# Kernel tuning notes

Measured on AMD Instinct MI355X. Metric: run time of the kernel, lower is better.

## Reference

```python
import jax, jax.numpy as jnp
import numpy as np

B, S, DM = 2, 2048, 2048
H, KV, HD = 16, 4, 128
THETA = 10000.0
EPS = 1e-6


def _rmsnorm(x, scale):
    # flax nnx.RMSNorm with dtype=float32: x / sqrt(mean(x^2)+eps) * scale
    var = jnp.mean(jnp.square(x.astype(jnp.float32)), axis=-1, keepdims=True)
    return (x.astype(jnp.float32) * jax.lax.rsqrt(var + EPS)) * scale


def _apply_rope(x, positions, base):
    # x: [B, S, heads, HD]; positions: [1, S]
    half = HD // 2
    fraction = 2.0 * jnp.arange(half, dtype=jnp.float32) / HD
    timescale = base ** fraction                              # [HD/2]
    sinusoid = positions[..., None].astype(jnp.float32) / timescale  # [1, S, HD/2]
    sinusoid = sinusoid[..., None, :]                         # [1, S, 1, HD/2]
    sin, cos = jnp.sin(sinusoid), jnp.cos(sinusoid)
    x1, x2 = x[..., :half], x[..., half:]
    return jnp.concatenate([x1 * cos - x2 * sin, x2 * cos + x1 * sin], axis=-1).astype(x.dtype)


def setup_inputs() -> dict:
    key = jax.random.key(0)
    ks = jax.random.split(key, 7)
    w = lambda k, shape: jax.random.normal(k, shape, jnp.float32) * 0.02
    return {
        "x": jax.random.normal(ks[0], (B, S, DM), jnp.float32),
        "wq": w(ks[1], (DM, H, HD)),
        "wk": w(ks[2], (DM, KV, HD)),
        "wv": w(ks[3], (DM, KV, HD)),
        "wo": w(ks[4], (H, HD, DM)),
        "q_scale": jnp.ones((HD,), jnp.float32),
        "k_scale": jnp.ones((HD,), jnp.float32),
    }


def reference(x, wq, wk, wv, wo, q_scale, k_scale):
    # QKV projections (LinearGeneral hidden -> (heads, head_dim))
    q = jnp.einsum("bsd,dhk->bshk", x, wq)   # [B,S,H,HD]
    k = jnp.einsum("bsd,dhk->bshk", x, wk)   # [B,S,KV,HD]
    v = jnp.einsum("bsd,dhk->bshk", x, wv)   # [B,S,KV,HD]
    # qk RMSNorm + cast back to compute dtype
    q = _rmsnorm(q, q_scale).astype(x.dtype)
    k = _rmsnorm(k, k_scale).astype(x.dtype)
    # RoPE
    positions = jnp.arange(S)[None, :]
    q = _apply_rope(q, positions, THETA)
    k = _apply_rope(k, positions, THETA)
    # GQA attention: group query heads per kv head instead of materializing repeat_kv
    G = H // KV
    qg = q.reshape(B, S, KV, G, HD) * (HD ** -0.5)
    scores = jnp.einsum("bqkgd,bskd->bkgqs", qg, k)           # [B,KV,G,S,S]
    causal = jnp.tril(jnp.ones((S, S), jnp.bool_))
    scores = jnp.where(causal, scores, jnp.finfo(scores.dtype).min)
    probs = jax.nn.softmax(scores, axis=-1)
    att = jnp.einsum("bkgqs,bskd->bqkgd", probs, v).reshape(B, S, H, HD)
    # output projection contracting (heads, head_dim)
    return jnp.einsum("bshd,hdo->bso", att, wo)
```

## Files before the change

### kernel.cpp

```cpp
#include <hip/hip_runtime.h>
#include <hip/hip_bf16.h>
#include <math.h>

typedef unsigned short u16;
typedef short short8 __attribute__((ext_vector_type(8)));
typedef float floatx4 __attribute__((ext_vector_type(4)));

#define B_   2
#define S_   2048
#define DM_  2048
#define H_   16
#define KVH_ 4
#define HD_  128

__device__ __forceinline__ float bf2f(u16 v) {
  union { unsigned int u; float f; } x; x.u = ((unsigned int)v) << 16; return x.f;
}
__device__ __forceinline__ u16 f2bf(float f) {
  union { float f; unsigned int u; } x; x.f = f;
  unsigned int u = x.u;
  u += 0x7FFFu + ((u >> 16) & 1u);
  return (u16)(u >> 16);
}

#define GLDS16(gp, lp) __builtin_amdgcn_global_load_lds( \
    (const __attribute__((address_space(1))) unsigned int*)(const void*)(gp), \
    (__attribute__((address_space(3))) unsigned int*)(void*)(lp), 16, 0, 0)

__global__ __launch_bounds__(256) void k_prep(
    const float* __restrict__ x, const float* __restrict__ wq,
    const float* __restrict__ wk, const float* __restrict__ wv,
    const float* __restrict__ wo,
    u16* __restrict__ x_bf, u16* __restrict__ wqkv_t, u16* __restrict__ wo_t)
{
  int bx = blockIdx.x;
  if (bx < 8192) {
    int i = bx * 256 + threadIdx.x;
    const float4 v = ((const float4*)x)[i];
    u16 o[4] = { f2bf(v.x), f2bf(v.y), f2bf(v.z), f2bf(v.w) };
    *(unsigned long long*)(x_bf + (size_t)i * 4) = *(unsigned long long*)o;
    return;
  }
  bx -= 8192;
  const float* src; u16* dst; int C, cb;
  if (bx < 4096)      { src = wq; dst = wqkv_t; C = 2048; cb = 64; }
  else if (bx < 5120) { bx -= 4096; src = wk; dst = wqkv_t + (size_t)2048 * 2048; C = 512; cb = 16; }
  else if (bx < 6144) { bx -= 5120; src = wv; dst = wqkv_t + (size_t)2560 * 2048; C = 512; cb = 16; }
  else                { bx -= 6144; src = wo; dst = wo_t; C = 2048; cb = 64; }
  const int R = 2048;
  int c0 = (bx % cb) * 32, r0 = (bx / cb) * 32;
  __shared__ float tile[32][33];
  int tx = threadIdx.x & 31, ty = threadIdx.x >> 5;
#pragma unroll
  for (int j = 0; j < 4; j++)
    tile[ty * 4 + j][tx] = src[(size_t)(r0 + ty * 4 + j) * C + c0 + tx];
  __syncthreads();
#pragma unroll
  for (int j = 0; j < 4; j++)
    dst[(size_t)(c0 + ty * 4 + j) * R + r0 + tx] = f2bf(tile[tx][ty * 4 + j]);
}

__global__ __launch_bounds__(256, 3) void k_gemm_bt(
    const u16* __restrict__ A, const u16* __restrict__ Bt,
    void* __restrict__ Cout, int M, int N, int K, int c_bf16)
{
  __shared__ u16 As[128 * 64];
  __shared__ u16 Bs[128 * 64];
  int tid = threadIdx.x;
  int lane = tid & 63;
  int quad = lane >> 4, l16 = lane & 15;
  int wid = tid >> 6;
  int m0 = blockIdx.y * 128, n0 = blockIdx.x * 128;
  int wm = (wid >> 1) * 64, wn = (wid & 1) * 64;

  floatx4 acc[4][4] = {};

  int srow = tid >> 3;
  int gjc0 = (tid & 7) ^ (srow & 7);
  const u16* Ap = A + (size_t)(m0 + srow) * K + gjc0 * 8;
  const u16* Bp = Bt + (size_t)(n0 + srow) * K + gjc0 * 8;
  u16* AsW = As + tid * 8;
  u16* BsW = Bs + tid * 8;

  for (int kt = 0; kt < K; kt += 64) {
    __syncthreads();
#pragma unroll
    for (int j = 0; j < 4; j++) {
      GLDS16(Ap + (size_t)(j * 32) * K, AsW + j * 2048);
      GLDS16(Bp + (size_t)(j * 32) * K, BsW + j * 2048);
    }
    Ap += 64; Bp += 64;
    __syncthreads();

#pragma unroll
    for (int ks = 0; ks < 2; ks++) {
      short8 af[4], bfv[4];
#pragma unroll
      for (int mi = 0; mi < 4; mi++) {
        int row = wm + mi * 16 + l16;
        af[mi] = *(const short8*)&As[row * 64 + (((ks * 4 + quad) ^ (row & 7)) * 8)];
      }
#pragma unroll
      for (int ni = 0; ni < 4; ni++) {
        int row = wn + ni * 16 + l16;
        bfv[ni] = *(const short8*)&Bs[row * 64 + (((ks * 4 + quad) ^ (row & 7)) * 8)];
      }
#pragma unroll
      for (int mi = 0; mi < 4; mi++)
#pragma unroll
        for (int ni = 0; ni < 4; ni++)
          acc[mi][ni] = __builtin_amdgcn_mfma_f32_16x16x32_bf16(
              af[mi], bfv[ni], acc[mi][ni], 0, 0, 0);
    }
  }

#pragma unroll
  for (int mi = 0; mi < 4; mi++)
#pragma unroll
    for (int ni = 0; ni < 4; ni++)
#pragma unroll
      for (int r = 0; r < 4; r++) {
        int row = m0 + wm + mi * 16 + quad * 4 + r;
        int col = n0 + wn + ni * 16 + l16;
        float v = acc[mi][ni][r];
        if (c_bf16) ((u16*)Cout)[(size_t)row * N + col] = f2bf(v);
        else        ((float*)Cout)[(size_t)row * N + col] = v;
      }
}

__global__ __launch_bounds__(256) void k_post(
    const u16* __restrict__ C1, const float* __restrict__ qs,
    const float* __restrict__ ks, u16* __restrict__ qr, u16* __restrict__ kr,
    u16* __restrict__ vt)
{
  int bx = blockIdx.x;
  if (bx < 4096) {
    int m = bx;
    int lane = threadIdx.x & 63, wid = threadIdx.x >> 6;
    int pos = m & (S_ - 1);
    float ts = powf(10000.0f, (float)lane * (1.0f / 64.0f));
    float ang = (float)pos / ts;
    float sn = sinf(ang), cs = cosf(ang);
    for (int r = wid; r < H_ + KVH_; r += 4) {
      bool isq = r < H_;
      const u16* src = C1 + (size_t)m * 3072 + (isq ? r * HD_ : DM_ + (r - H_) * HD_);
      float x1 = bf2f(src[lane]), x2 = bf2f(src[lane + 64]);
      float ss = x1 * x1 + x2 * x2;
#pragma unroll
      for (int d = 1; d < 64; d <<= 1) ss += __shfl_xor(ss, d);
      float rs = rsqrtf(ss * (1.0f / 128.0f) + 1e-6f);
      const float* sc = isq ? qs : ks;
      float y1 = x1 * rs * sc[lane];
      float y2 = x2 * rs * sc[lane + 64];
      float o1 = y1 * cs - y2 * sn;
      float o2 = y2 * cs + y1 * sn;
      if (isq) { o1 *= 0.088388347648318447f; o2 *= 0.088388347648318447f; }
      u16* dst = isq ? (qr + ((size_t)m * H_ + r) * HD_)
                     : (kr + ((size_t)m * KVH_ + (r - H_)) * HD_);
      dst[lane]      = f2bf(o1);
      dst[lane + 64] = f2bf(o2);
    }
    return;
  }
  bx -= 4096;
  int sx = bx & 63, rest = bx >> 6;
  int hy = rest & 3, bk = rest >> 2;
  int s0 = sx * 32, h0 = hy * 32;
  int b = bk >> 2, kv = bk & 3;
  __shared__ u16 tile[32][33];
  int tx = threadIdx.x & 31, ty = threadIdx.x >> 5;
#pragma unroll
  for (int j = 0; j < 4; j++)
    tile[ty * 4 + j][tx] =
        C1[(size_t)(b * S_ + s0 + ty * 4 + j) * 3072 + 2560 + kv * HD_ + h0 + tx];
  __syncthreads();
#pragma unroll
  for (int j = 0; j < 4; j++)
    vt[((size_t)bk * HD_ + h0 + ty * 4 + j) * S_ + s0 + tx] = tile[tx][ty * 4 + j];
}

__global__ __launch_bounds__(256, 2) void k_flash(
    const u16* __restrict__ qr, const u16* __restrict__ kr,
    const u16* __restrict__ vt, u16* __restrict__ att)
{
  __shared__ u16 Ks[64 * 128];
  __shared__ u16 Vt[128 * 64];
  __shared__ u16 Ps[4][32 * 64];
  int tid = threadIdx.x, lane = tid & 63, wid = tid >> 6;
  int quad = lane >> 4, l16 = lane & 15;
  int bx = blockIdx.x;
  int qi = 15 - (bx >> 5);
  int hb = bx & 31;
  int h = hb & 15, b = hb >> 4;
  int kvh = h >> 2;
  int q0 = qi * 128;
  int NT = 2 * qi + 2;
  int ktd = 2 * qi + (wid >> 1);

  short8 qf[2][4];
#pragma unroll
  for (int m = 0; m < 2; m++) {
    const u16* qb = qr + ((size_t)(b * S_ + q0 + wid * 32 + m * 16 + l16) * H_ + h) * HD_;
#pragma unroll
    for (int kk = 0; kk < 4; kk++)
      qf[m][kk] = *(const short8*)(qb + kk * 32 + quad * 8);
  }

  int gjk = (tid & 15) ^ ((tid >> 4) & 15);
  int gjv = (tid & 7) ^ ((tid >> 3) & 7);
  const u16* kp = kr + ((size_t)(b * S_ + (tid >> 4)) * KVH_ + kvh) * HD_ + gjk * 8;
  const u16* vp = vt + ((size_t)(b * KVH_ + kvh) * HD_ + (tid >> 3)) * S_ + gjv * 8;

  short8 pk[4], pv[4];
#pragma unroll
  for (int j = 0; j < 4; j++) {
    pk[j] = *(const short8*)(kp + (size_t)(j * 16) * KVH_ * HD_);
    pv[j] = *(const short8*)(vp + (size_t)(j * 32) * S_);
  }

  floatx4 accO[2][8] = {};
  float lp[2][4] = {};
  u16* PsW = &Ps[wid][0];

  const float LOG2E = 1.4426950408889634f;
  const float MBIAS = -12.5f * 1.4426950408889634f;

  for (int kt = 0; kt < NT; kt++) {
    int k0 = kt * 64;
#pragma unroll
    for (int j = 0; j < 4; j++) {
      *(short8*)&Ks[(j * 256 + tid) * 8] = pk[j];
      *(short8*)&Vt[(j * 256 + tid) * 8] = pv[j];
    }
    __syncthreads();

    if (kt + 1 < NT) {
      kp += (size_t)64 * KVH_ * HD_;
      vp += 64;
#pragma unroll
      for (int j = 0; j < 4; j++) {
        pk[j] = *(const short8*)(kp + (size_t)(j * 16) * KVH_ * HD_);
        pv[j] = *(const short8*)(vp + (size_t)(j * 32) * S_);
      }
    }

    if (kt <= ktd) {
      floatx4 sacc[2][4] = {};
      __builtin_amdgcn_s_setprio(1);
#pragma unroll
      for (int kk = 0; kk < 4; kk++) {
        short8 kf[4];
#pragma unroll
        for (int nt = 0; nt < 4; nt++) {
          int row = nt * 16 + l16;
          kf[nt] = *(const short8*)&Ks[row * 128 + (((kk * 4 + quad) ^ (row & 15)) * 8)];
        }
#pragma unroll
        for (int nt = 0; nt < 4; nt++) {
          sacc[0][nt] = __builtin_amdgcn_mfma_f32_16x16x32_bf16(qf[0][kk], kf[nt], sacc[0][nt], 0, 0, 0);
          sacc[1][nt] = __builtin_amdgcn_mfma_f32_16x16x32_bf16(qf[1][kk], kf[nt], sacc[1][nt], 0, 0, 0);
        }
      }
      __builtin_amdgcn_s_setprio(0);

      bool diag = (kt == ktd);
#pragma unroll
      for (int m = 0; m < 2; m++)
#pragma unroll
        for (int r = 0; r < 4; r++) {
          int prow = m * 16 + quad * 4 + r;
          int qrow = q0 + wid * 32 + prow;
          float rsum = 0.f;
#pragma unroll
          for (int nt = 0; nt < 4; nt++) {
            float p = __builtin_amdgcn_exp2f(fmaf(sacc[m][nt][r], LOG2E, MBIAS));
            if (diag && (k0 + nt * 16 + l16) > qrow) p = 0.f;
            rsum += p;
            PsW[prow * 64 + (((nt * 2 + (l16 >> 3)) ^ (prow & 7)) * 8) + (l16 & 7)] = f2bf(p);
          }
          lp[m][r] += rsum;
        }

      __builtin_amdgcn_s_setprio(1);
#pragma unroll
      for (int kk = 0; kk < 2; kk++) {
        short8 pf[2];
#pragma unroll
        for (int m = 0; m < 2; m++) {
          int prow = m * 16 + l16;
          pf[m] = *(const short8*)&PsW[prow * 64 + (((kk * 4 + quad) ^ (prow & 7)) * 8)];
        }
#pragma unroll
        for (int ht = 0; ht < 8; ht++) {
          int row = ht * 16 + l16;
          short8 vf = *(const short8*)&Vt[row * 64 + (((kk * 4 + quad) ^ (row & 7)) * 8)];
          accO[0][ht] = __builtin_amdgcn_mfma_f32_16x16x32_bf16(pf[0], vf, accO[0][ht], 0, 0, 0);
          accO[1][ht] = __builtin_amdgcn_mfma_f32_16x16x32_bf16(pf[1], vf, accO[1][ht], 0, 0, 0);
        }
      }
      __builtin_amdgcn_s_setprio(0);
    }
    __syncthreads();
  }

#pragma unroll
  for (int m = 0; m < 2; m++)
#pragma unroll
    for (int r = 0; r < 4; r++) {
#pragma unroll
      for (int d = 1; d < 16; d <<= 1) lp[m][r] += __shfl_xor(lp[m][r], d);
      lp[m][r] = 1.0f / lp[m][r];
    }

#pragma unroll
  for (int m = 0; m < 2; m++)
#pragma unroll
    for (int ht = 0; ht < 8; ht++)
#pragma unroll
      for (int r = 0; r < 4; r++) {
        int row = q0 + wid * 32 + m * 16 + quad * 4 + r;
        att[((size_t)(b * S_ + row) * H_ + h) * HD_ + ht * 16 + l16] =
            f2bf(accO[m][ht][r] * lp[m][r]);
      }
}

extern "C" void kernel_launch(void* const* d_in, const int* in_sizes, int n_in,
                              void* d_out, int out_size, void* d_ws, size_t ws_size,
                              hipStream_t stream)
{
  const float* x  = (const float*)d_in[0];
  const float* wq = (const float*)d_in[1];
  const float* wk = (const float*)d_in[2];
  const float* wv = (const float*)d_in[3];
  const float* wo = (const float*)d_in[4];
  const float* qs = (const float*)d_in[5];
  const float* ks = (const float*)d_in[6];

  char* ws = (char*)d_ws;
  size_t off = 0;
  u16* x_bf   = (u16*)(ws + off); off += (size_t)4096 * 2048 * 2;
  u16* wqkv_t = (u16*)(ws + off); off += (size_t)3072 * 2048 * 2;
  u16* wo_t   = (u16*)(ws + off); off += (size_t)2048 * 2048 * 2;
  u16* C1     = (u16*)(ws + off); off += (size_t)4096 * 3072 * 2;
  u16* q_rope = (u16*)(ws + off); off += (size_t)4096 * 16 * 128 * 2;
  u16* k_rope = (u16*)(ws + off); off += (size_t)4096 * 4 * 128 * 2;
  u16* vt     = (u16*)(ws + off); off += (size_t)8 * 128 * 2048 * 2;
  u16* att    = (u16*)(ws + off); off += (size_t)4096 * 2048 * 2;

  k_prep<<<dim3(18432), 256, 0, stream>>>(x, wq, wk, wv, wo, x_bf, wqkv_t, wo_t);

  k_gemm_bt<<<dim3(24, 32), 256, 0, stream>>>(x_bf, wqkv_t, C1, 4096, 3072, 2048, 1);

  k_post<<<dim3(6144), 256, 0, stream>>>(C1, qs, ks, q_rope, k_rope, vt);

  k_flash<<<dim3(512), 256, 0, stream>>>(q_rope, k_rope, vt, att);

  k_gemm_bt<<<dim3(16, 32), 256, 0, stream>>>(att, wo_t, d_out, 4096, 2048, 2048, 0);

  (void)in_sizes; (void)n_in; (void)out_size; (void)ws_size;
}
```

Before: 302.9 us.

## Split flash key tiles across wave pairs with double-buffered direct-to-LDS loads

The attention kernel now processes 64-row query tiles, giving twice as many blocks. The four waves split into two row halves by two key halves, and the split-K partial outputs and row sums are combined through shared memory at the end. K/V tiles are loaded with GLDS16 (global-to-LDS) into double buffers instead of through register staging, which removes one barrier per iteration. This aims at better load balance and occupancy across CUs and at hiding load latency, at the cost of more LDS and a final cross-wave reduction.

```diff
diff --git a/kernel.cpp b/kernel.cpp
--- a/kernel.cpp
+++ b/kernel.cpp
@@ -183,24 +183,26 @@
     const u16* __restrict__ qr, const u16* __restrict__ kr,
     const u16* __restrict__ vt, u16* __restrict__ att)
 {
-  __shared__ u16 Ks[64 * 128];
-  __shared__ u16 Vt[128 * 64];
-  __shared__ u16 Ps[4][32 * 64];
+  __shared__ u16 smem[39168] __attribute__((aligned(16)));
+  u16* Ps = smem + 32768;
+  float* lpbuf = (float*)(smem + 38912);
+
   int tid = threadIdx.x, lane = tid & 63, wid = tid >> 6;
   int quad = lane >> 4, l16 = lane & 15;
+  int rhalf = wid & 1;
+  int shalf = wid >> 1;
   int bx = blockIdx.x;
-  int qi = 15 - (bx >> 5);
+  int it = 31 - (bx >> 5);
   int hb = bx & 31;
   int h = hb & 15, b = hb >> 4;
   int kvh = h >> 2;
-  int q0 = qi * 128;
-  int NT = 2 * qi + 2;
-  int ktd = 2 * qi + (wid >> 1);
+  int q0 = it * 64;
+  int NT = it + 1;
 
   short8 qf[2][4];
 #pragma unroll
   for (int m = 0; m < 2; m++) {
-    const u16* qb = qr + ((size_t)(b * S_ + q0 + wid * 32 + m * 16 + l16) * H_ + h) * HD_;
+    const u16* qb = qr + ((size_t)(b * S_ + q0 + rhalf * 32 + m * 16 + l16) * H_ + h) * HD_;
 #pragma unroll
     for (int kk = 0; kk < 4; kk++)
       qf[m][kk] = *(const short8*)(qb + kk * 32 + quad * 8);
@@ -211,117 +213,145 @@
   const u16* kp = kr + ((size_t)(b * S_ + (tid >> 4)) * KVH_ + kvh) * HD_ + gjk * 8;
   const u16* vp = vt + ((size_t)(b * KVH_ + kvh) * HD_ + (tid >> 3)) * S_ + gjv * 8;
 
-  short8 pk[4], pv[4];
 #pragma unroll
   for (int j = 0; j < 4; j++) {
-    pk[j] = *(const short8*)(kp + (size_t)(j * 16) * KVH_ * HD_);
-    pv[j] = *(const short8*)(vp + (size_t)(j * 32) * S_);
-  }
+    GLDS16(kp + (size_t)(j * 16) * KVH_ * HD_, smem + (size_t)(j * 256 + tid) * 8);
+    GLDS16(vp + (size_t)(j * 32) * S_,         smem + 16384 + (size_t)(j * 256 + tid) * 8);
+  }
+  kp += (size_t)64 * KVH_ * HD_;
+  vp += 64;
+  __syncthreads();
 
   floatx4 accO[2][8] = {};
   float lp[2][4] = {};
-  u16* PsW = &Ps[wid][0];
+  u16* PsW = Ps + wid * 1536;
 
   const float LOG2E = 1.4426950408889634f;
   const float MBIAS = -12.5f * 1.4426950408889634f;
+  int qmax = q0 + rhalf * 32 + 31;
 
   for (int kt = 0; kt < NT; kt++) {
-    int k0 = kt * 64;
-#pragma unroll
-    for (int j = 0; j < 4; j++) {
-      *(short8*)&Ks[(j * 256 + tid) * 8] = pk[j];
-      *(short8*)&Vt[(j * 256 + tid) * 8] = pv[j];
-    }
-    __syncthreads();
-
     if (kt + 1 < NT) {
+      u16* KD = smem + (size_t)((kt + 1) & 1) * 8192;
+      u16* VD = smem + 16384 + (size_t)((kt + 1) & 1) * 8192;
+#pragma unroll
+      for (int j = 0; j < 4; j++) {
+        GLDS16(kp + (size_t)(j * 16) * KVH_ * HD_, KD + (size_t)(j * 256 + tid) * 8);
+        GLDS16(vp + (size_t)(j * 32) * S_,         VD + (size_t)(j * 256 + tid) * 8);
+      }
       kp += (size_t)64 * KVH_ * HD_;
       vp += 64;
-#pragma unroll
-      for (int j = 0; j < 4; j++) {
-        pk[j] = *(const short8*)(kp + (size_t)(j * 16) * KVH_ * HD_);
-        pv[j] = *(const short8*)(vp + (size_t)(j * 32) * S_);
-      }
-    }
-
-    if (kt <= ktd) {
-      floatx4 sacc[2][4] = {};
+    }
+
+    int k0 = kt * 64;
+    int s0w = k0 + shalf * 32;
+    if (s0w <= qmax) {
+      const u16* KsC = smem + (size_t)(kt & 1) * 8192;
+      const u16* VtC = smem + 16384 + (size_t)(kt & 1) * 8192;
+
+      floatx4 sacc[2][2] = {};
       __builtin_amdgcn_s_setprio(1);
 #pragma unroll
       for (int kk = 0; kk < 4; kk++) {
-        short8 kf[4];
-#pragma unroll
-        for (int nt = 0; nt < 4; nt++) {
-          int row = nt * 16 + l16;
-          kf[nt] = *(const short8*)&Ks[row * 128 + (((kk * 4 + quad) ^ (row & 15)) * 8)];
+        short8 kf[2];
+#pragma unroll
+        for (int nt = 0; nt < 2; nt++) {
+          int row = shalf * 32 + nt * 16 + l16;
+          kf[nt] = *(const short8*)&KsC[row * 128 + (((kk * 4 + quad) ^ (row & 15)) * 8)];
         }
 #pragma unroll
-        for (int nt = 0; nt < 4; nt++) {
+        for (int nt = 0; nt < 2; nt++) {
           sacc[0][nt] = __builtin_amdgcn_mfma_f32_16x16x32_bf16(qf[0][kk], kf[nt], sacc[0][nt], 0, 0, 0);
           sacc[1][nt] = __builtin_amdgcn_mfma_f32_16x16x32_bf16(qf[1][kk], kf[nt], sacc[1][nt], 0, 0, 0);
         }
       }
       __builtin_amdgcn_s_setprio(0);
 
-      bool diag = (kt == ktd);
+      bool diag = (s0w + 31 > q0 + rhalf * 32);
 #pragma unroll
       for (int m = 0; m < 2; m++)
 #pragma unroll
         for (int r = 0; r < 4; r++) {
           int prow = m * 16 + quad * 4 + r;
-          int qrow = q0 + wid * 32 + prow;
+          int qrow = q0 + rhalf * 32 + prow;
           float rsum = 0.f;
 #pragma unroll
-          for (int nt = 0; nt < 4; nt++) {
+          for (int nt = 0; nt < 2; nt++) {
             float p = __builtin_amdgcn_exp2f(fmaf(sacc[m][nt][r], LOG2E, MBIAS));
-            if (diag && (k0 + nt * 16 + l16) > qrow) p = 0.f;
+            if (diag && (s0w + nt * 16 + l16) > qrow) p = 0.f;
             rsum += p;
-            PsW[prow * 64 + (((nt * 2 + (l16 >> 3)) ^ (prow & 7)) * 8) + (l16 & 7)] = f2bf(p);
+            int chunk = nt * 2 + (l16 >> 3);
+            PsW[prow * 48 + ((chunk ^ (quad & 1)) * 8) + (l16 & 7)] = f2bf(p);
           }
           lp[m][r] += rsum;
         }
 
       __builtin_amdgcn_s_setprio(1);
-#pragma unroll
-      for (int kk = 0; kk < 2; kk++) {
-        short8 pf[2];
-#pragma unroll
-        for (int m = 0; m < 2; m++) {
-          int prow = m * 16 + l16;
-          pf[m] = *(const short8*)&PsW[prow * 64 + (((kk * 4 + quad) ^ (prow & 7)) * 8)];
+      short8 pf[2];
+#pragma unroll
+      for (int m = 0; m < 2; m++) {
+        int prow = m * 16 + l16;
+        pf[m] = *(const short8*)&PsW[prow * 48 + ((quad ^ ((l16 >> 2) & 1)) * 8)];
+      }
+#pragma unroll
+      for (int ht = 0; ht < 8; ht++) {
+        int row = ht * 16 + l16;
+        short8 vf = *(const short8*)&VtC[row * 64 + (((shalf * 4 + quad) ^ (row & 7)) * 8)];
+        accO[0][ht] = __builtin_amdgcn_mfma_f32_16x16x32_bf16(pf[0], vf, accO[0][ht], 0, 0, 0);
+        accO[1][ht] = __builtin_amdgcn_mfma_f32_16x16x32_bf16(pf[1], vf, accO[1][ht], 0, 0, 0);
+      }
+      __builtin_amdgcn_s_setprio(0);
+    }
+    __syncthreads();
+  }
+
+#pragma unroll
+  for (int m = 0; m < 2; m++)
+#pragma unroll
+    for (int r = 0; r < 4; r++) {
+#pragma unroll
+      for (int d = 1; d < 16; d <<= 1) lp[m][r] += __shfl_xor(lp[m][r], d);
+    }
+
+  floatx4* xch = (floatx4*)(void*)smem;
+  if (wid >= 2) {
+    floatx4* dst = xch + ((wid & 1) * 1024 + lane * 16);
+#pragma unroll
+    for (int m = 0; m < 2; m++)
+#pragma unroll
+      for (int ht = 0; ht < 8; ht++) dst[m * 8 + ht] = accO[m][ht];
+    if (l16 == 0) {
+#pragma unroll
+      for (int m = 0; m < 2; m++)
+#pragma unroll
+        for (int r = 0; r < 4; r++)
+          lpbuf[(wid & 1) * 32 + m * 16 + quad * 4 + r] = lp[m][r];
+    }
+  }
+  __syncthreads();
+  if (wid < 2) {
+    floatx4* src = xch + (wid * 1024 + lane * 16);
+    float inv[2][4];
+#pragma unroll
+    for (int m = 0; m < 2; m++)
+#pragma unroll
+      for (int ht = 0; ht < 8; ht++) accO[m][ht] += src[m * 8 + ht];
+#pragma unroll
+    for (int m = 0; m < 2; m++)
+#pragma unroll
+      for (int r = 0; r < 4; r++)
+        inv[m][r] = 1.0f / (lp[m][r] + lpbuf[wid * 32 + m * 16 + quad * 4 + r]);
+#pragma unroll
+    for (int m = 0; m < 2; m++)
+#pragma unroll
+      for (int ht = 0; ht < 8; ht++)
+#pragma unroll
+        for (int r = 0; r < 4; r++) {
+          int row = q0 + wid * 32 + m * 16 + quad * 4 + r;
+          att[((size_t)(b * S_ + row) * H_ + h) * HD_ + ht * 16 + l16] =
+              f2bf(accO[m][ht][r] * inv[m][r]);
         }
-#pragma unroll
-        for (int ht = 0; ht < 8; ht++) {
-          int row = ht * 16 + l16;
-          short8 vf = *(const short8*)&Vt[row * 64 + (((kk * 4 + quad) ^ (row & 7)) * 8)];
-          accO[0][ht] = __builtin_amdgcn_mfma_f32_16x16x32_bf16(pf[0], vf, accO[0][ht], 0, 0, 0);
-          accO[1][ht] = __builtin_amdgcn_mfma_f32_16x16x32_bf16(pf[1], vf, accO[1][ht], 0, 0, 0);
-        }
-      }
-      __builtin_amdgcn_s_setprio(0);
-    }
-    __syncthreads();
-  }
-
-#pragma unroll
-  for (int m = 0; m < 2; m++)
-#pragma unroll
-    for (int r = 0; r < 4; r++) {
-#pragma unroll
-      for (int d = 1; d < 16; d <<= 1) lp[m][r] += __shfl_xor(lp[m][r], d);
-      lp[m][r] = 1.0f / lp[m][r];
-    }
-
-#pragma unroll
-  for (int m = 0; m < 2; m++)
-#pragma unroll
-    for (int ht = 0; ht < 8; ht++)
-#pragma unroll
-      for (int r = 0; r < 4; r++) {
-        int row = q0 + wid * 32 + m * 16 + quad * 4 + r;
-        att[((size_t)(b * S_ + row) * H_ + h) * HD_ + ht * 16 + l16] =
-            f2bf(accO[m][ht][r] * lp[m][r]);
-      }
+  }
 }
 
 extern "C" void kernel_launch(void* const* d_in, const int* in_sizes, int n_in,
@@ -353,7 +383,7 @@
 
   k_post<<<dim3(6144), 256, 0, stream>>>(C1, qs, ks, q_rope, k_rope, vt);
 
-  k_flash<<<dim3(512), 256, 0, stream>>>(q_rope, k_rope, vt, att);
+  k_flash<<<dim3(1024), 256, 0, stream>>>(q_rope, k_rope, vt, att);
 
   k_gemm_bt<<<dim3(16, 32), 256, 0, stream>>>(att, wo_t, d_out, 4096, 2048, 2048, 0);
 
```

After: 290.9 us. 4.0% less time.
